# Kernel optimization log

Hardware: AMD Instinct MI355X
Metric: run time of the kernel (lower is better)

The kernel has to match this reference:

```python
import jax, jax.numpy as jnp
import numpy as np
from jax.scipy.special import erf

# synthetic covalent radii table (original imports `covalent_radii`, e.g. from ase)
COV_RADII = jnp.asarray(0.3 + 0.02 * np.arange(100), dtype=jnp.float32)

B_MOL = 1024   # molecules per batch
N_ATOM = 128   # atoms per molecule (equal-sized ragged batch, atoms sorted by molecule)
N_ELEM = 10


def setup_inputs() -> dict:
    key = jax.random.key(0)
    ks = jax.random.split(key, 6)
    N = B_MOL * N_ATOM
    return {
        "eneg": jax.random.normal(ks[0], (N, 1), jnp.float32),
        "positions": jax.random.normal(ks[1], (N, 3), jnp.float32) * 3.0,
        "node_attrs": jax.random.uniform(ks[2], (N, N_ELEM), jnp.float32),
        "hardness": jax.random.uniform(ks[3], (N_ELEM,), jnp.float32),
        "total_charge": jax.random.normal(ks[4], (B_MOL,), jnp.float32),
        "batch": jnp.repeat(jnp.arange(B_MOL), N_ATOM),          # sorted molecule ids
        "atomic_numbers": jax.random.randint(ks[5], (N,), 1, 90),
    }


def reference(eneg, positions, node_attrs, hardness, total_charge, batch, atomic_numbers):
    # atoms are sorted by molecule with equal molecule sizes, so the ragged
    # python loop of the original collapses to a batched [B, n, ...] computation.
    B = total_charge.shape[0]
    N = positions.shape[0]
    n = N // B
    sqrt_pi = jnp.sqrt(jnp.asarray(np.pi, jnp.float32))
    sqrt_2 = jnp.sqrt(jnp.asarray(2.0, jnp.float32))

    pos = positions.reshape(B, n, 3)
    Z = atomic_numbers.reshape(B, n)
    atom_idx = jnp.argmax(node_attrs, axis=1).reshape(B, n)

    r = COV_RADII[Z]                                     # [B, n]
    diag_vals = hardness[atom_idx] + 1.0 / (sqrt_pi * r)  # [B, n]
    sigma = jnp.square(r)                                # [B, n]
    gamma = jnp.sqrt(sigma[:, :, None] + sigma[:, None, :])  # [B, n, n]

    diff = pos[:, :, None, :] - pos[:, None, :, :]       # [B, n, n, 3]
    sq = jnp.sum(diff * diff, axis=-1)                   # [B, n, n]
    eye = jnp.eye(n, dtype=bool)
    dist = jnp.sqrt(jnp.where(eye, 1.0, sq))             # safe diag (overwritten below)

    A = erf(dist / (sqrt_2 * gamma)) / dist              # [B, n, n]
    A = jnp.where(eye, diag_vals[:, :, None], A)         # scatter hardness diagonal

    # augment with charge-conservation row/column of ones (corner = 1)
    A = jnp.concatenate([A, jnp.ones((B, n, 1), A.dtype)], axis=2)
    A = jnp.concatenate([A, jnp.ones((B, 1, n + 1), A.dtype)], axis=1)

    b = jnp.concatenate([-eneg.reshape(B, n, 1),
                         total_charge.reshape(B, 1, 1)], axis=1)  # [B, n+1, 1]

    x = jnp.linalg.solve(A, b)                           # batched small solves
    return x[:, :n, 0].reshape(-1)                       # partial charges, [N]
```

## Files before the change

kernel.cpp:

```cpp
#include <hip/hip_runtime.h>
#include <math.h>

#define NMOL  1024
#define N     128
#define NELEM 10
#define BLOCK 256
#define PW    8
#define NPAN  16
#define PSTR  12
#define USTR  132

typedef __attribute__((ext_vector_type(4))) float f4;


__global__ __launch_bounds__(BLOCK, 2) void ceq_solve_kernel(
    const float* __restrict__ eneg,
    const float* __restrict__ positions,
    const float* __restrict__ node_attrs,
    const float* __restrict__ hardness,
    const float* __restrict__ total_charge,
    const int*   __restrict__ atomic_numbers,
    float* __restrict__ out)
{
    __shared__ __align__(16) float P[2][N * PSTR];
    __shared__ __align__(16) float Up[2][PW * USTR];
    __shared__ __align__(16) float Ublk[2][NPAN][PW][PW];
    __shared__ float Dinv[2][PW], Dd[2][PW];
    __shared__ float rhsY[2][N], rhsZ[2][N];
    __shared__ float sxY[2][N], sxZ[2][N];
    __shared__ float px[2][N], py[2][N], pz[2][N], sg[2][N], dgv[2][N];
    __shared__ float lamS[2];

    const int tid  = threadIdx.x;
    const int lane = tid & 63;
    const int g    = tid >> 7;
    const int gt   = tid & 127;
    const int wv   = (tid >> 6) & 1;
    const int r0   = 2 * lane;
    const int r1   = r0 + 1;
    const int col0 = 64 * wv;
    const int mol  = 2 * blockIdx.x + g;
    const int base = mol * N;

    {
        const int i = gt;
        const int Z = atomic_numbers[base + i];
        const float rad = 0.3f + 0.02f * (float)Z;
        sg[g][i] = rad * rad;
        const float* na = node_attrs + (size_t)(base + i) * NELEM;
        float best = na[0]; int bi = 0;
        #pragma unroll
        for (int e = 1; e < NELEM; ++e) {
            float v = na[e];
            if (v > best) { best = v; bi = e; }
        }
        dgv[g][i] = hardness[bi] + 0.5641895835477563f / rad;
        const float* p = positions + (size_t)(base + i) * 3;
        px[g][i] = p[0]; py[g][i] = p[1]; pz[g][i] = p[2];
        rhsY[g][i] = -eneg[base + i];
        rhsZ[g][i] = 1.0f;
    }
    __syncthreads();

    f4 Ar0[16], Ar1[16];
    {
        const float x0 = px[g][r0], y0 = py[g][r0], z0 = pz[g][r0];
        const float s0 = sg[g][r0], d0 = dgv[g][r0];
        #pragma unroll
        for (int c = 0; c < 16; ++c) {
            f4 v0;
            #pragma unroll
            for (int e = 0; e < 4; ++e) {
                const int j = col0 + 4 * c + e;
                float a0;
                if (j == r0) a0 = d0;
                else {
                    const float dx = x0 - px[g][j], dy = y0 - py[g][j], dz = z0 - pz[g][j];
                    const float d = sqrtf(dx * dx + dy * dy + dz * dz);
                    a0 = erff(d / (1.4142135623730951f * sqrtf(s0 + sg[g][j]))) / d;
                }
                ((float*)&v0)[e] = a0;
            }
            Ar0[c] = v0;
        }
        const float x1 = px[g][r1], y1 = py[g][r1], z1 = pz[g][r1];
        const float s1 = sg[g][r1], d1 = dgv[g][r1];
        #pragma unroll
        for (int c = 0; c < 16; ++c) {
            f4 v1;
            #pragma unroll
            for (int e = 0; e < 4; ++e) {
                const int j = col0 + 4 * c + e;
                float a1;
                if (j == r1) a1 = d1;
                else {
                    const float dx = x1 - px[g][j], dy = y1 - py[g][j], dz = z1 - pz[g][j];
                    const float d = sqrtf(dx * dx + dy * dy + dz * dz);
                    a1 = erff(d / (1.4142135623730951f * sqrtf(s1 + sg[g][j]))) / d;
                }
                ((float*)&v1)[e] = a1;
            }
            Ar1[c] = v1;
        }
    }

    for (int p = 0; p < NPAN; ++p) {
        const int k0   = PW * p;
        const int gclo = 2 * p + 2;
        const int q    = p & 7;

        if (wv == (p >> 3) && lane >= 4 * p) {
            f4 a00, a01, a10, a11;
            switch (q) {
                case 0:  a00 = Ar0[0];  a01 = Ar0[1];  a10 = Ar1[0];  a11 = Ar1[1];  break;
                case 1:  a00 = Ar0[2];  a01 = Ar0[3];  a10 = Ar1[2];  a11 = Ar1[3];  break;
                case 2:  a00 = Ar0[4];  a01 = Ar0[5];  a10 = Ar1[4];  a11 = Ar1[5];  break;
                case 3:  a00 = Ar0[6];  a01 = Ar0[7];  a10 = Ar1[6];  a11 = Ar1[7];  break;
                case 4:  a00 = Ar0[8];  a01 = Ar0[9];  a10 = Ar1[8];  a11 = Ar1[9];  break;
                case 5:  a00 = Ar0[10]; a01 = Ar0[11]; a10 = Ar1[10]; a11 = Ar1[11]; break;
                case 6:  a00 = Ar0[12]; a01 = Ar0[13]; a10 = Ar1[12]; a11 = Ar1[13]; break;
                default: a00 = Ar0[14]; a01 = Ar0[15]; a10 = Ar1[14]; a11 = Ar1[15]; break;
            }
            if (lane >= 4 * p + 4) {
                *(f4*)&P[g][r0 * PSTR + 0] = a00; *(f4*)&P[g][r0 * PSTR + 4] = a01;
                *(f4*)&P[g][r1 * PSTR + 0] = a10; *(f4*)&P[g][r1 * PSTR + 4] = a11;
            } else {
                float u0[PW] = { a00.x, a00.y, a00.z, a00.w, a01.x, a01.y, a01.z, a01.w };
                float u1[PW] = { a10.x, a10.y, a10.z, a10.w, a11.x, a11.y, a11.z, a11.w };
                float ry0 = rhsY[g][r0], rz0 = rhsZ[g][r0];
                float ry1 = rhsY[g][r1], rz1 = rhsZ[g][r1];
                const int rl = lane - 4 * p;
                #pragma unroll
                for (int kk = 0; kk < PW; ++kk) {
                    const int src = 4 * p + (kk >> 1);
                    float pr[PW];
                    #pragma unroll
                    for (int j = kk; j < PW; ++j)
                        pr[j] = __shfl((kk & 1) ? u1[j] : u0[j], src);
                    const float cY = __shfl((kk & 1) ? ry1 : ry0, src);
                    const float cZ = __shfl((kk & 1) ? rz1 : rz0, src);
                    const float dinv = 1.0f / pr[kk];
                    if (2 * rl > kk) {
                        const float m = u0[kk] * dinv; u0[kk] = m;
                        #pragma unroll
                        for (int j = kk + 1; j < PW; ++j) u0[j] -= m * pr[j];
                        ry0 -= m * cY; rz0 -= m * cZ;
                    }
                    if (2 * rl + 1 > kk) {
                        const float m = u1[kk] * dinv; u1[kk] = m;
                        #pragma unroll
                        for (int j = kk + 1; j < PW; ++j) u1[j] -= m * pr[j];
                        ry1 -= m * cY; rz1 -= m * cZ;
                    }
                    if (rl == (kk >> 1)) { Dinv[g][kk] = dinv; Dd[g][kk] = pr[kk]; }
                }
                f4 w0 = { u0[0], u0[1], u0[2], u0[3] }, w1 = { u0[4], u0[5], u0[6], u0[7] };
                *(f4*)&Ublk[g][p][2 * rl][0] = w0; *(f4*)&Ublk[g][p][2 * rl][4] = w1;
                f4 w2 = { u1[0], u1[1], u1[2], u1[3] }, w3 = { u1[4], u1[5], u1[6], u1[7] };
                *(f4*)&Ublk[g][p][2 * rl + 1][0] = w2; *(f4*)&Ublk[g][p][2 * rl + 1][4] = w3;
                rhsY[g][r0] = ry0; rhsZ[g][r0] = rz0;
                rhsY[g][r1] = ry1; rhsZ[g][r1] = rz1;
            }
        }
        __syncthreads();

        const int nb = (N - PW) - k0;
        if (gt < nb) {
            const int i = k0 + PW + gt;
            f4 a = *(const f4*)&P[g][i * PSTR], b = *(const f4*)&P[g][i * PSTR + 4];
            float av[PW] = { a.x, a.y, a.z, a.w, b.x, b.y, b.z, b.w };
            float m[PW];
            #pragma unroll
            for (int j = 0; j < PW; ++j) {
                float acc = av[j];
                #pragma unroll
                for (int t = 0; t < j; ++t) acc -= m[t] * Ublk[g][p][t][j];
                m[j] = acc * Dinv[g][j];
            }
            f4 ma = { m[0], m[1], m[2], m[3] }, mb = { m[4], m[5], m[6], m[7] };
            *(f4*)&P[g][i * PSTR]     = ma;
            *(f4*)&P[g][i * PSTR + 4] = mb;
            #pragma unroll
            for (int u = 0; u < PW; ++u) Up[g][u * USTR + i] = m[u] * Dd[g][u];
            float ry = rhsY[g][i], rz = rhsZ[g][i];
            #pragma unroll
            for (int t = 0; t < PW; ++t) {
                ry -= m[t] * rhsY[g][k0 + t];
                rz -= m[t] * rhsZ[g][k0 + t];
            }
            rhsY[g][i] = ry; rhsZ[g][i] = rz;
        }
        __syncthreads();

        if (lane >= 4 * p && lane < 4 * p + 4) {
            const int u0 = r0 - k0, u1 = u0 + 1;
            #pragma unroll
            for (int c = 0; c < 16; ++c) {
                const int gc = 16 * wv + c;
                if (gc >= gclo) {
                    Ar0[c] = *(const f4*)&Up[g][u0 * USTR + 4 * gc];
                    Ar1[c] = *(const f4*)&Up[g][u1 * USTR + 4 * gc];
                }
            }
        }
        const bool hasmat = (16 * wv + 15) >= gclo;
        if (hasmat && lane >= 4 * p + 4) {
            float lA0[PW], lA1[PW];
            {
                f4 a = *(const f4*)&P[g][r0 * PSTR], b = *(const f4*)&P[g][r0 * PSTR + 4];
                lA0[0]=a.x; lA0[1]=a.y; lA0[2]=a.z; lA0[3]=a.w;
                lA0[4]=b.x; lA0[5]=b.y; lA0[6]=b.z; lA0[7]=b.w;
                f4 c2 = *(const f4*)&P[g][r1 * PSTR], d2 = *(const f4*)&P[g][r1 * PSTR + 4];
                lA1[0]=c2.x; lA1[1]=c2.y; lA1[2]=c2.z; lA1[3]=c2.w;
                lA1[4]=d2.x; lA1[5]=d2.y; lA1[6]=d2.z; lA1[7]=d2.w;
            }
            #pragma unroll
            for (int c = 0; c < 16; ++c) {
                const int gc = 16 * wv + c;
                if (gc >= gclo) {
                    f4 acc0 = Ar0[c], acc1 = Ar1[c];
                    #pragma unroll
                    for (int u = 0; u < PW; ++u) {
                        const f4 uv = *(const f4*)&Up[g][u * USTR + 4 * gc];
                        acc0 -= uv * lA0[u];
                        acc1 -= uv * lA1[u];
                    }
                    Ar0[c] = acc0; Ar1[c] = acc1;
                }
            }
        }
        __syncthreads();
    }

    for (int pb = NPAN - 1; pb >= 0; --pb) {
        const int k0 = PW * pb;
        if (tid < 4) {
            const int gg = tid >> 1;
            float* rhs = (tid & 1) ? rhsZ[gg] : rhsY[gg];
            float* sx  = (tid & 1) ? sxZ[gg]  : sxY[gg];
            float x[PW];
            #pragma unroll
            for (int kk = PW - 1; kk >= 0; --kk) {
                float acc = rhs[k0 + kk];
                #pragma unroll
                for (int jj = kk + 1; jj < PW; ++jj) acc -= Ublk[gg][pb][kk][jj] * x[jj];
                x[kk] = acc / Ublk[gg][pb][kk][kk];
                sx[k0 + kk] = x[kk];
            }
        }
        __syncthreads();
        if (wv == (pb >> 3) && lane < 4 * pb) {
            f4 a00, a01, a10, a11;
            switch (pb & 7) {
                case 0:  a00 = Ar0[0];  a01 = Ar0[1];  a10 = Ar1[0];  a11 = Ar1[1];  break;
                case 1:  a00 = Ar0[2];  a01 = Ar0[3];  a10 = Ar1[2];  a11 = Ar1[3];  break;
                case 2:  a00 = Ar0[4];  a01 = Ar0[5];  a10 = Ar1[4];  a11 = Ar1[5];  break;
                case 3:  a00 = Ar0[6];  a01 = Ar0[7];  a10 = Ar1[6];  a11 = Ar1[7];  break;
                case 4:  a00 = Ar0[8];  a01 = Ar0[9];  a10 = Ar1[8];  a11 = Ar1[9];  break;
                case 5:  a00 = Ar0[10]; a01 = Ar0[11]; a10 = Ar1[10]; a11 = Ar1[11]; break;
                case 6:  a00 = Ar0[12]; a01 = Ar0[13]; a10 = Ar1[12]; a11 = Ar1[13]; break;
                default: a00 = Ar0[14]; a01 = Ar0[15]; a10 = Ar1[14]; a11 = Ar1[15]; break;
            }
            float yy0 = rhsY[g][r0], yy1 = rhsY[g][r1];
            float zz0 = rhsZ[g][r0], zz1 = rhsZ[g][r1];
            yy0 -= a00.x*sxY[g][k0]   + a00.y*sxY[g][k0+1] + a00.z*sxY[g][k0+2] + a00.w*sxY[g][k0+3]
                 + a01.x*sxY[g][k0+4] + a01.y*sxY[g][k0+5] + a01.z*sxY[g][k0+6] + a01.w*sxY[g][k0+7];
            yy1 -= a10.x*sxY[g][k0]   + a10.y*sxY[g][k0+1] + a10.z*sxY[g][k0+2] + a10.w*sxY[g][k0+3]
                 + a11.x*sxY[g][k0+4] + a11.y*sxY[g][k0+5] + a11.z*sxY[g][k0+6] + a11.w*sxY[g][k0+7];
            zz0 -= a00.x*sxZ[g][k0]   + a00.y*sxZ[g][k0+1] + a00.z*sxZ[g][k0+2] + a00.w*sxZ[g][k0+3]
                 + a01.x*sxZ[g][k0+4] + a01.y*sxZ[g][k0+5] + a01.z*sxZ[g][k0+6] + a01.w*sxZ[g][k0+7];
            zz1 -= a10.x*sxZ[g][k0]   + a10.y*sxZ[g][k0+1] + a10.z*sxZ[g][k0+2] + a10.w*sxZ[g][k0+3]
                 + a11.x*sxZ[g][k0+4] + a11.y*sxZ[g][k0+5] + a11.z*sxZ[g][k0+6] + a11.w*sxZ[g][k0+7];
            rhsY[g][r0] = yy0; rhsY[g][r1] = yy1;
            rhsZ[g][r0] = zz0; rhsZ[g][r1] = zz1;
        }
        __syncthreads();
    }

    if (wv == 0) {
        float vY = sxY[g][lane] + sxY[g][lane + 64];
        float vZ = sxZ[g][lane] + sxZ[g][lane + 64];
        #pragma unroll
        for (int off = 32; off; off >>= 1) {
            vY += __shfl_xor(vY, off);
            vZ += __shfl_xor(vZ, off);
        }
        if (lane == 0) lamS[g] = (vY - total_charge[mol]) / (vZ - 1.0f);
    }
    __syncthreads();
    out[base + gt] = sxY[g][gt] - lamS[g] * sxZ[g][gt];
}

extern "C" void kernel_launch(void* const* d_in, const int* in_sizes, int n_in,
                              void* d_out, int out_size, void* d_ws, size_t ws_size,
                              hipStream_t stream) {
    const float* eneg           = (const float*)d_in[0];
    const float* positions      = (const float*)d_in[1];
    const float* node_attrs     = (const float*)d_in[2];
    const float* hardness       = (const float*)d_in[3];
    const float* total_charge   = (const float*)d_in[4];
    const int*   atomic_numbers = (const int*)d_in[6];
    float* out = (float*)d_out;

    ceq_solve_kernel<<<NMOL / 2, BLOCK, 0, stream>>>(
        eneg, positions, node_attrs, hardness, total_charge, atomic_numbers, out);
}
```

Baseline: 224.2 us.

## Interleave column panels across the two wavefronts to balance LU work

Changes the column ownership from contiguous halves (wave 0 owns columns 0-63, wave 1 owns 64-127) to interleaved 8-column panels alternating between the two wavefronts. Under the old split, wave 0 ran out of trailing-update work after the first eight panels while wave 1 kept working through all sixteen. With the interleaved layout both waves keep updating panels throughout the factorization. It also merges the two row-generation loops into one, which may raise register pressure.

```diff
diff --git a/kernel.cpp b/kernel.cpp
--- a/kernel.cpp
+++ b/kernel.cpp
@@ -38,7 +38,6 @@
     const int wv   = (tid >> 6) & 1;
     const int r0   = 2 * lane;
     const int r1   = r0 + 1;
-    const int col0 = 64 * wv;
     const int mol  = 2 * blockIdx.x + g;
     const int base = mol * N;
 
@@ -66,50 +65,41 @@
     {
         const float x0 = px[g][r0], y0 = py[g][r0], z0 = pz[g][r0];
         const float s0 = sg[g][r0], d0 = dgv[g][r0];
+        const float x1 = px[g][r1], y1 = py[g][r1], z1 = pz[g][r1];
+        const float s1 = sg[g][r1], d1 = dgv[g][r1];
         #pragma unroll
         for (int c = 0; c < 16; ++c) {
-            f4 v0;
+            const int jb = 16 * (c >> 1) + 8 * wv + 4 * (c & 1);
+            f4 v0, v1;
             #pragma unroll
             for (int e = 0; e < 4; ++e) {
-                const int j = col0 + 4 * c + e;
-                float a0;
+                const int j = jb + e;
+                float a0, a1;
                 if (j == r0) a0 = d0;
                 else {
                     const float dx = x0 - px[g][j], dy = y0 - py[g][j], dz = z0 - pz[g][j];
                     const float d = sqrtf(dx * dx + dy * dy + dz * dz);
                     a0 = erff(d / (1.4142135623730951f * sqrtf(s0 + sg[g][j]))) / d;
                 }
-                ((float*)&v0)[e] = a0;
-            }
-            Ar0[c] = v0;
-        }
-        const float x1 = px[g][r1], y1 = py[g][r1], z1 = pz[g][r1];
-        const float s1 = sg[g][r1], d1 = dgv[g][r1];
-        #pragma unroll
-        for (int c = 0; c < 16; ++c) {
-            f4 v1;
-            #pragma unroll
-            for (int e = 0; e < 4; ++e) {
-                const int j = col0 + 4 * c + e;
-                float a1;
                 if (j == r1) a1 = d1;
                 else {
                     const float dx = x1 - px[g][j], dy = y1 - py[g][j], dz = z1 - pz[g][j];
                     const float d = sqrtf(dx * dx + dy * dy + dz * dz);
                     a1 = erff(d / (1.4142135623730951f * sqrtf(s1 + sg[g][j]))) / d;
                 }
+                ((float*)&v0)[e] = a0;
                 ((float*)&v1)[e] = a1;
             }
+            Ar0[c] = v0;
             Ar1[c] = v1;
         }
     }
 
     for (int p = 0; p < NPAN; ++p) {
-        const int k0   = PW * p;
-        const int gclo = 2 * p + 2;
-        const int q    = p & 7;
-
-        if (wv == (p >> 3) && lane >= 4 * p) {
+        const int k0 = PW * p;
+        const int q  = (p >> 1) & 7;
+
+        if (wv == (p & 1) && lane >= 4 * p) {
             f4 a00, a01, a10, a11;
             switch (q) {
                 case 0:  a00 = Ar0[0];  a01 = Ar0[1];  a10 = Ar1[0];  a11 = Ar1[1];  break;
@@ -196,14 +186,15 @@
             const int u0 = r0 - k0, u1 = u0 + 1;
             #pragma unroll
             for (int c = 0; c < 16; ++c) {
-                const int gc = 16 * wv + c;
-                if (gc >= gclo) {
+                const int t  = 2 * (c >> 1) + wv;
+                const int gc = 4 * (c >> 1) + 2 * wv + (c & 1);
+                if (t > p) {
                     Ar0[c] = *(const f4*)&Up[g][u0 * USTR + 4 * gc];
                     Ar1[c] = *(const f4*)&Up[g][u1 * USTR + 4 * gc];
                 }
             }
         }
-        const bool hasmat = (16 * wv + 15) >= gclo;
+        const bool hasmat = (14 + wv) > p;
         if (hasmat && lane >= 4 * p + 4) {
             float lA0[PW], lA1[PW];
             {
@@ -216,8 +207,9 @@
             }
             #pragma unroll
             for (int c = 0; c < 16; ++c) {
-                const int gc = 16 * wv + c;
-                if (gc >= gclo) {
+                const int t  = 2 * (c >> 1) + wv;
+                const int gc = 4 * (c >> 1) + 2 * wv + (c & 1);
+                if (t > p) {
                     f4 acc0 = Ar0[c], acc1 = Ar1[c];
                     #pragma unroll
                     for (int u = 0; u < PW; ++u) {
@@ -249,9 +241,9 @@
             }
         }
         __syncthreads();
-        if (wv == (pb >> 3) && lane < 4 * pb) {
+        if (wv == (pb & 1) && lane < 4 * pb) {
             f4 a00, a01, a10, a11;
-            switch (pb & 7) {
+            switch ((pb >> 1) & 7) {
                 case 0:  a00 = Ar0[0];  a01 = Ar0[1];  a10 = Ar1[0];  a11 = Ar1[1];  break;
                 case 1:  a00 = Ar0[2];  a01 = Ar0[3];  a10 = Ar1[2];  a11 = Ar1[3];  break;
                 case 2:  a00 = Ar0[4];  a01 = Ar0[5];  a10 = Ar1[4];  a11 = Ar1[5];  break;
```

New measurement: 214.5 us. -4.3%, faster.
